# Optimization experiments

Measured on AMD Instinct MI355X. Metric: run time of the kernel, lower is better.

Reference implementation:

```python
import jax, jax.numpy as jnp
import numpy as np
import math

B, S, D = 2, 4096, 512
H = 8
DH = D // H  # 64


def setup_inputs() -> dict:
    key = jax.random.key(0)
    k1, k2, k3, k4, k5 = jax.random.split(key, 5)
    scale = 1.0 / math.sqrt(D)
    return {
        "x": jax.random.normal(k1, (B, S, D), dtype=jnp.float32),
        "W_in": jax.random.normal(k2, (D, 3 * D), dtype=jnp.float32) * scale,
        "b_in": jax.random.normal(k3, (3 * D,), dtype=jnp.float32) * 0.01,
        "W_out": jax.random.normal(k4, (D, D), dtype=jnp.float32) * scale,
        "b_out": jax.random.normal(k5, (D,), dtype=jnp.float32) * 0.01,
        "causal_mask": 1,
    }


def reference(x, W_in, b_in, W_out, b_out, causal_mask):
    b, s, d = x.shape
    # fused QKV projection: (b, s, 3d)
    qkv = x @ W_in + b_in
    q, k, v = jnp.split(qkv, 3, axis=-1)
    # (b, s, d) -> (b, h, s, dh)
    def to_heads(t):
        return t.reshape(b, s, H, DH).transpose(0, 2, 1, 3)
    q, k, v = to_heads(q), to_heads(k), to_heads(v)
    # raw scores (b, h, s, s)
    scores = jnp.einsum("bhqd,bhkd->bhqk", q, k)
    if causal_mask:  # static python flag
        # upper-triangular (strictly above diag) -> -inf, applied pre-scaling
        # (matches source; -inf invariant under /sqrt(d_head))
        tri = jnp.triu(jnp.ones((s, s), dtype=bool), k=1)
        scores = jnp.where(tri, -jnp.inf, scores)
    attn = jax.nn.softmax(scores / math.sqrt(DH), axis=-1)
    out = jnp.einsum("bhqk,bhkd->bhqd", attn, v)
    out = out.transpose(0, 2, 1, 3).reshape(b, s, d)
    return out @ W_out + b_out
```

## Files before the change

### kernel.cpp

```cpp
#include <hip/hip_runtime.h>
#include <cstdint>
#include <cmath>

typedef unsigned short BF16;
typedef __attribute__((ext_vector_type(8))) short short8;
typedef __attribute__((ext_vector_type(4))) float f32x4;
typedef __attribute__((ext_vector_type(16))) float f32x16;
typedef __attribute__((ext_vector_type(2))) unsigned int uint2v;
typedef __attribute__((ext_vector_type(4))) unsigned int uint4v;

#define S_LEN 4096
#define DMODEL 512
#define NHEAD 8
#define DHEAD 64
#define BS 2
#define NROWS (BS * NHEAD * S_LEN)

__device__ __forceinline__ BF16 f2bf(float f) {
  union { float f; uint32_t u; } v; v.f = f;
  uint32_t r = (v.u + 0x7FFFu + ((v.u >> 16) & 1u)) >> 16;
  return (BF16)r;
}

__device__ __forceinline__ unsigned cvtpk(float a, float b) {
  unsigned r;
  asm volatile("v_cvt_pk_bf16_f32 %0, %1, %2" : "=v"(r) : "v"(a), "v"(b));
  return r;
}

__device__ __forceinline__ float partner32(float x, int hi) {
  unsigned a = __float_as_uint(x), b = a;
  uint2v r = __builtin_amdgcn_permlane32_swap(a, b, false, false);
  return __uint_as_float(hi ? r[0] : r[1]);
}

__device__ __forceinline__ void pl32(unsigned &a, unsigned &b) {
  uint2v r = __builtin_amdgcn_permlane32_swap(a, b, false, false);
  a = r[0]; b = r[1];
}

__device__ __forceinline__ void gload16(const void* g, void* lds) {
  __builtin_amdgcn_global_load_lds(
      (const __attribute__((address_space(1))) void*)g,
      (__attribute__((address_space(3))) void*)lds, 16, 0, 0);
}

#define MAX3(a, b, c) fmaxf(fmaxf((a), (b)), (c))
#define CS_CONST 0.18033688011112042f

__global__ __launch_bounds__(256) void cvt_x_k(const float* __restrict__ x,
                                               BF16* __restrict__ xb) {
  int i = blockIdx.x * 256 + threadIdx.x;
  float4 v = reinterpret_cast<const float4*>(x)[i];
  ushort4 o;
  o.x = f2bf(v.x); o.y = f2bf(v.y); o.z = f2bf(v.z); o.w = f2bf(v.w);
  reinterpret_cast<ushort4*>(xb)[i] = o;
}

__global__ __launch_bounds__(256) void tr_cvt_k(const float* __restrict__ W,
                                                BF16* __restrict__ Wt,
                                                int K, int N) {
  __shared__ float t[32][33];
  int n0 = blockIdx.x * 32, k0 = blockIdx.y * 32;
  int tx = threadIdx.x & 31, ty = threadIdx.x >> 5;
#pragma unroll
  for (int i = 0; i < 4; ++i)
    t[ty + 8 * i][tx] = W[(size_t)(k0 + ty + 8 * i) * N + n0 + tx];
  __syncthreads();
#pragma unroll
  for (int i = 0; i < 4; ++i)
    Wt[(size_t)(n0 + ty + 8 * i) * K + k0 + tx] = f2bf(t[tx][ty + 8 * i]);
}

template <int MODE>
__global__ __launch_bounds__(256)
void gemm_k(const BF16* __restrict__ A, const BF16* __restrict__ Bt,
            const float* __restrict__ bias,
            BF16* __restrict__ Qb, BF16* __restrict__ Kb, BF16* __restrict__ Vt,
            float* __restrict__ Out) {
  __shared__ BF16 As[128 * 64];
  __shared__ BF16 Bs[128 * 64];
  const int tid = threadIdx.x;
  const int l = tid & 63, w = tid >> 6;
  const int wm = w >> 1, wn = w & 1;
  const int bm = blockIdx.x, bn = blockIdx.y;
  f32x4 acc[4][4] = {};

  for (int kt = 0; kt < 512 / 64; ++kt) {
#pragma unroll
    for (int i = 0; i < 4; ++i) {
      int ldsoff = i * 4096 + w * 1024;
      int off = ldsoff + l * 16;
      int row = off >> 7;
      int slot = ((off >> 4) & 7) ^ (row & 7);
      gload16(A + (size_t)(bm * 128 + row) * 512 + kt * 64 + slot * 8,
              (char*)As + ldsoff);
      gload16(Bt + (size_t)(bn * 128 + row) * 512 + kt * 64 + slot * 8,
              (char*)Bs + ldsoff);
    }
    __syncthreads();
    const char* Ab = (const char*)As;
    const char* Bb = (const char*)Bs;
    short8 af[4][2], bfr[4][2];
#pragma unroll
    for (int mf = 0; mf < 4; ++mf)
#pragma unroll
      for (int kk = 0; kk < 2; ++kk) {
        int row = wm * 64 + mf * 16 + (l & 15);
        int slot = ((l >> 4) + 4 * kk) ^ (row & 7);
        af[mf][kk] = *(const short8*)(Ab + row * 128 + slot * 16);
      }
#pragma unroll
    for (int nf = 0; nf < 4; ++nf)
#pragma unroll
      for (int kk = 0; kk < 2; ++kk) {
        int row = wn * 64 + nf * 16 + (l & 15);
        int slot = ((l >> 4) + 4 * kk) ^ (row & 7);
        bfr[nf][kk] = *(const short8*)(Bb + row * 128 + slot * 16);
      }
    __builtin_amdgcn_s_setprio(1);
#pragma unroll
    for (int kk = 0; kk < 2; ++kk)
#pragma unroll
      for (int mf = 0; mf < 4; ++mf)
#pragma unroll
        for (int nf = 0; nf < 4; ++nf)
          acc[mf][nf] = __builtin_amdgcn_mfma_f32_16x16x32_bf16(
              af[mf][kk], bfr[nf][kk], acc[mf][nf], 0, 0, 0);
    __builtin_amdgcn_s_setprio(0);
    __syncthreads();
  }

#pragma unroll
  for (int mf = 0; mf < 4; ++mf)
#pragma unroll
    for (int nf = 0; nf < 4; ++nf)
#pragma unroll
      for (int r = 0; r < 4; ++r) {
        int row = bm * 128 + wm * 64 + mf * 16 + ((l >> 4) << 2) + r;
        int col = bn * 128 + wn * 64 + nf * 16 + (l & 15);
        float v = acc[mf][nf][r] + bias[col];
        if (MODE == 0) {
          int sec = col >> 9, nl = col & 511;
          int h = nl >> 6, dh = nl & 63;
          int b = row >> 12, s = row & 4095;
          size_t bh = (size_t)(b * NHEAD + h);
          if (sec == 0)
            Qb[(bh * S_LEN + s) * DHEAD + dh] = f2bf(v);
          else if (sec == 1)
            Kb[(bh * S_LEN + s) * DHEAD + dh] = f2bf(v);
          else
            Vt[(bh * DHEAD + dh) * S_LEN + s] = f2bf(v);
        } else {
          Out[(size_t)row * DMODEL + col] = v;
        }
      }
}

__global__ __launch_bounds__(256, 2)
void attn_k(const BF16* __restrict__ Qg, const BF16* __restrict__ Kg,
            const BF16* __restrict__ Vg, float* __restrict__ Op0,
            float* __restrict__ Op1, float* __restrict__ Ml) {
  __shared__ BF16 Kl[2][64 * 64];
  __shared__ BF16 Vl[2][64 * 64];
  const int tid = threadIdx.x, l = tid & 63, w = tid >> 6;
  const int hi = l >> 5, ln = l & 31;
  const int wgid = blockIdx.x;
  const int xcd = wgid & 7, j = wgid >> 3;
  const int bh = xcd * 2 + (j & 1);
  const int half = (j >> 1) & 1;
  const int p = j >> 2;
  const BF16* Qh = Qg + (size_t)bh * S_LEN * DHEAD;
  const BF16* Kh = Kg + (size_t)bh * S_LEN * DHEAD;
  const BF16* Vh = Vg + (size_t)bh * DHEAD * S_LEN;
  const float CS = CS_CONST;

  int cur = 0;
  for (int rep = 0; rep < 2; ++rep) {
    const int qt = rep ? (31 - p) : p;
    const int kbase = half ? (qt + 1) : 0;
    const int NT = qt + 1;
    const int q0w = qt * 128 + w * 32;
    const int qrow = q0w + ln;
    __syncthreads();

    short8 qb[4];
    {
      const BF16* qp = Qh + (size_t)qrow * DHEAD + hi * 8;
#pragma unroll
      for (int ks = 0; ks < 4; ++ks) qb[ks] = *(const short8*)(qp + ks * 16);
    }
    f32x16 oacc0 = {}, oacc1 = {};
    float m_ = -INFINITY, l_ = 0.f;

    auto stage = [&](int buf, int ktile) {
      const int kv0 = ktile * 64;
#pragma unroll
      for (int i = 0; i < 2; ++i) {
        int base = i * 4096 + w * 1024;
        int off = base + l * 16;
        int row = off >> 7;
        int slot = ((off >> 4) & 7) ^ (row & 7);
        gload16(Kh + (size_t)(kv0 + row) * DHEAD + slot * 8, (char*)Kl[buf] + base);
        gload16(Vh + (size_t)row * S_LEN + kv0 + slot * 8, (char*)Vl[buf] + base);
      }
    };
    stage(cur, kbase);

    for (int kt = 0; kt < NT; ++kt) {
      __syncthreads();
      if (kt + 1 < NT) stage(cur ^ 1, kbase + kt + 1);
      const int kv0 = (kbase + kt) * 64;
      if (kv0 <= q0w + 31) {
        const char* Kb_ = (const char*)Kl[cur];
        f32x16 s0 = {}, s1 = {};
        __builtin_amdgcn_s_setprio(1);
#pragma unroll
        for (int ks = 0; ks < 4; ++ks) {
          int slot0 = (2 * ks + hi) ^ (ln & 7);
          short8 kf0 = *(const short8*)(Kb_ + ln * 128 + slot0 * 16);
          int row1 = 32 + ln;
          int slot1 = (2 * ks + hi) ^ (row1 & 7);
          short8 kf1 = *(const short8*)(Kb_ + row1 * 128 + slot1 * 16);
          s0 = __builtin_amdgcn_mfma_f32_32x32x16_bf16(kf0, qb[ks], s0, 0, 0, 0);
          s1 = __builtin_amdgcn_mfma_f32_32x32x16_bf16(kf1, qb[ks], s1, 0, 0, 0);
        }
        __builtin_amdgcn_s_setprio(0);
        if (kv0 + 63 > q0w) {
#pragma unroll
          for (int r = 0; r < 16; ++r) {
            int crow = (r & 3) + 8 * (r >> 2) + 4 * hi;
            if (kv0 + crow > qrow) s0[r] = -INFINITY;
            if (kv0 + 32 + crow > qrow) s1[r] = -INFINITY;
          }
        }
        float a0 = MAX3(s0[0], s0[1], s0[2]);
        float a1 = MAX3(s0[3], s0[4], s0[5]);
        float a2 = MAX3(s0[6], s0[7], s0[8]);
        float a3 = MAX3(s0[9], s0[10], s0[11]);
        float a4 = MAX3(s0[12], s0[13], s0[14]);
        float a5 = MAX3(s0[15], s1[0], s1[1]);
        float a6 = MAX3(s1[2], s1[3], s1[4]);
        float a7 = MAX3(s1[5], s1[6], s1[7]);
        float a8 = MAX3(s1[8], s1[9], s1[10]);
        float a9 = MAX3(s1[11], s1[12], s1[13]);
        float a10 = fmaxf(s1[14], s1[15]);
        float b0 = MAX3(a0, a1, a2);
        float b1 = MAX3(a3, a4, a5);
        float b2 = MAX3(a6, a7, a8);
        float b3 = fmaxf(a9, a10);
        float pmax = fmaxf(fmaxf(b0, b1), fmaxf(b2, b3));
        pmax = fmaxf(pmax, partner32(pmax, hi));
        bool need = (pmax - m_) * CS > 8.0f;
        if (__any(need)) {
          float mn = fmaxf(m_, pmax);
          float alpha = exp2f((m_ - mn) * CS);
          m_ = mn;
          l_ *= alpha;
#pragma unroll
          for (int r = 0; r < 16; ++r) { oacc0[r] *= alpha; oacc1[r] *= alpha; }
        }
        const float mb = m_ * CS;
        float p0[16], p1[16];
        float rs = 0.f;
#pragma unroll
        for (int r = 0; r < 16; ++r) { p0[r] = exp2f(fmaf(s0[r], CS, -mb)); rs += p0[r]; }
#pragma unroll
        for (int r = 0; r < 16; ++r) { p1[r] = exp2f(fmaf(s1[r], CS, -mb)); rs += p1[r]; }
        rs += partner32(rs, hi);
        l_ += rs;
        short8 pf[4];
#pragma unroll
        for (int hf = 0; hf < 2; ++hf) {
          const float* pp = hf ? p1 : p0;
          unsigned w01 = cvtpk(pp[0], pp[1]), w23 = cvtpk(pp[2], pp[3]);
          unsigned w45 = cvtpk(pp[4], pp[5]), w67 = cvtpk(pp[6], pp[7]);
          unsigned w89 = cvtpk(pp[8], pp[9]), wab = cvtpk(pp[10], pp[11]);
          unsigned wcd = cvtpk(pp[12], pp[13]), wef = cvtpk(pp[14], pp[15]);
          pl32(w01, w45);
          pl32(w23, w67);
          pl32(w89, wcd);
          pl32(wab, wef);
          union { uint4v u; short8 s; } c0, c1;
          c0.u = (uint4v){w01, w23, w45, w67};
          c1.u = (uint4v){w89, wab, wcd, wef};
          pf[hf * 2 + 0] = c0.s;
          pf[hf * 2 + 1] = c1.s;
        }
        const char* Vb_ = (const char*)Vl[cur];
        __builtin_amdgcn_s_setprio(1);
#pragma unroll
        for (int ks = 0; ks < 4; ++ks) {
          int slot0 = (2 * ks + hi) ^ (ln & 7);
          short8 vf0 = *(const short8*)(Vb_ + ln * 128 + slot0 * 16);
          int row1 = 32 + ln;
          int slot1 = (2 * ks + hi) ^ (row1 & 7);
          short8 vf1 = *(const short8*)(Vb_ + row1 * 128 + slot1 * 16);
          oacc0 = __builtin_amdgcn_mfma_f32_32x32x16_bf16(vf0, pf[ks], oacc0, 0, 0, 0);
          oacc1 = __builtin_amdgcn_mfma_f32_32x32x16_bf16(vf1, pf[ks], oacc1, 0, 0, 0);
        }
        __builtin_amdgcn_s_setprio(0);
      }
      cur ^= 1;
    }

    float* Op = half ? Op1 : Op0;
    const size_t rowbase = ((size_t)bh * S_LEN + qrow) * DHEAD;
#pragma unroll
    for (int blk = 0; blk < 2; ++blk) {
      const f32x16 oa = blk ? oacc1 : oacc0;
#pragma unroll
      for (int g = 0; g < 4; ++g) {
        int dh0 = 8 * g + 4 * hi + 32 * blk;
        float4 st = {oa[4 * g + 0], oa[4 * g + 1], oa[4 * g + 2], oa[4 * g + 3]};
        *(float4*)(Op + rowbase + dh0) = st;
      }
    }
    if (hi == 0) {
      float2 ml = {m_, l_};
      *(float2*)(Ml + ((size_t)half * NROWS + (size_t)bh * S_LEN + qrow) * 2) = ml;
    }
  }
}

__global__ __launch_bounds__(256)
void merge_k(const float* __restrict__ Op0, const float* __restrict__ Op1,
             const float* __restrict__ Ml, BF16* __restrict__ Ob) {
  const int wv = blockIdx.x * 4 + (threadIdx.x >> 6);
  const int lane = threadIdx.x & 63;
  const int row0 = wv * 64;
  for (int r = 0; r < 64; ++r) {
    int row = row0 + r;
    float2 ml1 = *(const float2*)(Ml + (size_t)row * 2);
    float2 ml2 = *(const float2*)(Ml + ((size_t)NROWS + row) * 2);
    float m = fmaxf(ml1.x, ml2.x);
    float a1 = exp2f((ml1.x - m) * CS_CONST);
    float a2 = exp2f((ml2.x - m) * CS_CONST);
    float linv = 1.0f / (ml1.y * a1 + ml2.y * a2);
    float o = (Op0[(size_t)row * 64 + lane] * a1 +
               Op1[(size_t)row * 64 + lane] * a2) * linv;
    int bh = row >> 12, s = row & 4095;
    Ob[((size_t)((bh >> 3) * S_LEN + s)) * DMODEL + (bh & 7) * DHEAD + lane] = f2bf(o);
  }
}

extern "C" void kernel_launch(void* const* d_in, const int* in_sizes, int n_in,
                              void* d_out, int out_size, void* d_ws, size_t ws_size,
                              hipStream_t stream) {
  const float* x = (const float*)d_in[0];
  const float* W_in = (const float*)d_in[1];
  const float* b_in = (const float*)d_in[2];
  const float* W_out = (const float*)d_in[3];
  const float* b_out = (const float*)d_in[4];
  float* out = (float*)d_out;

  char* ws = (char*)d_ws;
  const size_t SZ_X = (size_t)BS * S_LEN * DMODEL * 2;
  const size_t SZ_OP = (size_t)NROWS * DHEAD * 4;
  BF16* xb    = (BF16*)(ws);
  BF16* wint  = (BF16*)(ws + SZ_X);
  BF16* woutt = (BF16*)(ws + SZ_X + 3 * DMODEL * DMODEL * 2);
  BF16* Qb    = (BF16*)(ws + SZ_X + 4 * DMODEL * DMODEL * 2);
  BF16* Kb    = (BF16*)((char*)Qb + SZ_X);
  BF16* Vt    = (BF16*)((char*)Kb + SZ_X);
  BF16* Ob    = (BF16*)((char*)Vt + SZ_X);
  float* Op0  = (float*)((char*)Ob + SZ_X);
  float* Op1  = (float*)((char*)Op0 + SZ_OP);
  float* Ml   = (float*)((char*)Op1 + SZ_OP);

  cvt_x_k<<<dim3((BS * S_LEN * DMODEL) / 4 / 256), 256, 0, stream>>>(x, xb);
  tr_cvt_k<<<dim3(3 * DMODEL / 32, DMODEL / 32), 256, 0, stream>>>(W_in, wint, DMODEL, 3 * DMODEL);
  tr_cvt_k<<<dim3(DMODEL / 32, DMODEL / 32), 256, 0, stream>>>(W_out, woutt, DMODEL, DMODEL);
  gemm_k<0><<<dim3(BS * S_LEN / 128, 3 * DMODEL / 128), 256, 0, stream>>>(
      xb, wint, b_in, Qb, Kb, Vt, nullptr);
  attn_k<<<dim3(512), 256, 0, stream>>>(Qb, Kb, Vt, Op0, Op1, Ml);
  merge_k<<<dim3(256), 256, 0, stream>>>(Op0, Op1, Ml, Ob);
  gemm_k<1><<<dim3(BS * S_LEN / 128, DMODEL / 128), 256, 0, stream>>>(
      Ob, woutt, b_out, nullptr, nullptr, nullptr, out);
}
```

Baseline: 209.4 us.

## Split attention KV range four ways, store bf16 partials, raise occupancy

Attention work per query tile is now split over four KV ranges instead of two, doubling the grid to 1024 workgroups and raising the launch-bounds occupancy hint to 4. Partial outputs are stored as bf16 instead of fp32, and the merge kernel combines four partials using their per-slice max and sum. The aim is better load balance and more parallelism across CUs, plus less partial-output traffic. In exchange there are more Q reloads and partial writes, added merge work, bf16 rounding of unnormalized partials, and possible register pressure or spills under the tighter occupancy bound.

```diff
diff --git a/kernel.cpp b/kernel.cpp
--- a/kernel.cpp
+++ b/kernel.cpp
@@ -157,10 +157,10 @@
       }
 }
 
-__global__ __launch_bounds__(256, 2)
+__global__ __launch_bounds__(256, 4)
 void attn_k(const BF16* __restrict__ Qg, const BF16* __restrict__ Kg,
-            const BF16* __restrict__ Vg, float* __restrict__ Op0,
-            float* __restrict__ Op1, float* __restrict__ Ml) {
+            const BF16* __restrict__ Vg, BF16* __restrict__ Opb,
+            float* __restrict__ Ml) {
   __shared__ BF16 Kl[2][64 * 64];
   __shared__ BF16 Vl[2][64 * 64];
   const int tid = threadIdx.x, l = tid & 63, w = tid >> 6;
@@ -168,8 +168,8 @@
   const int wgid = blockIdx.x;
   const int xcd = wgid & 7, j = wgid >> 3;
   const int bh = xcd * 2 + (j & 1);
-  const int half = (j >> 1) & 1;
-  const int p = j >> 2;
+  const int qr = (j >> 1) & 3;
+  const int p = j >> 3;
   const BF16* Qh = Qg + (size_t)bh * S_LEN * DHEAD;
   const BF16* Kh = Kg + (size_t)bh * S_LEN * DHEAD;
   const BF16* Vh = Vg + (size_t)bh * DHEAD * S_LEN;
@@ -178,8 +178,11 @@
   int cur = 0;
   for (int rep = 0; rep < 2; ++rep) {
     const int qt = rep ? (31 - p) : p;
-    const int kbase = half ? (qt + 1) : 0;
-    const int NT = qt + 1;
+    const int qq = rep ? (3 - qr) : qr;
+    const int NTf = 2 * qt + 2;
+    const int kbase = (qq * NTf) >> 2;
+    const int kend = ((qq + 1) * NTf) >> 2;
+    const int NT = kend - kbase;
     const int q0w = qt * 128 + w * 32;
     const int qrow = q0w + ln;
     __syncthreads();
@@ -205,140 +208,153 @@
         gload16(Vh + (size_t)row * S_LEN + kv0 + slot * 8, (char*)Vl[buf] + base);
       }
     };
-    stage(cur, kbase);
-
-    for (int kt = 0; kt < NT; ++kt) {
-      __syncthreads();
-      if (kt + 1 < NT) stage(cur ^ 1, kbase + kt + 1);
-      const int kv0 = (kbase + kt) * 64;
-      if (kv0 <= q0w + 31) {
-        const char* Kb_ = (const char*)Kl[cur];
-        f32x16 s0 = {}, s1 = {};
-        __builtin_amdgcn_s_setprio(1);
-#pragma unroll
-        for (int ks = 0; ks < 4; ++ks) {
-          int slot0 = (2 * ks + hi) ^ (ln & 7);
-          short8 kf0 = *(const short8*)(Kb_ + ln * 128 + slot0 * 16);
-          int row1 = 32 + ln;
-          int slot1 = (2 * ks + hi) ^ (row1 & 7);
-          short8 kf1 = *(const short8*)(Kb_ + row1 * 128 + slot1 * 16);
-          s0 = __builtin_amdgcn_mfma_f32_32x32x16_bf16(kf0, qb[ks], s0, 0, 0, 0);
-          s1 = __builtin_amdgcn_mfma_f32_32x32x16_bf16(kf1, qb[ks], s1, 0, 0, 0);
+
+    if (NT > 0) {
+      stage(cur, kbase);
+      for (int kt = 0; kt < NT; ++kt) {
+        __syncthreads();
+        if (kt + 1 < NT) stage(cur ^ 1, kbase + kt + 1);
+        const int kv0 = (kbase + kt) * 64;
+        if (kv0 <= q0w + 31) {
+          const char* Kb_ = (const char*)Kl[cur];
+          f32x16 s0 = {}, s1 = {};
+          __builtin_amdgcn_s_setprio(1);
+#pragma unroll
+          for (int ks = 0; ks < 4; ++ks) {
+            int slot0 = (2 * ks + hi) ^ (ln & 7);
+            short8 kf0 = *(const short8*)(Kb_ + ln * 128 + slot0 * 16);
+            int row1 = 32 + ln;
+            int slot1 = (2 * ks + hi) ^ (row1 & 7);
+            short8 kf1 = *(const short8*)(Kb_ + row1 * 128 + slot1 * 16);
+            s0 = __builtin_amdgcn_mfma_f32_32x32x16_bf16(kf0, qb[ks], s0, 0, 0, 0);
+            s1 = __builtin_amdgcn_mfma_f32_32x32x16_bf16(kf1, qb[ks], s1, 0, 0, 0);
+          }
+          __builtin_amdgcn_s_setprio(0);
+          if (kv0 + 63 > q0w) {
+#pragma unroll
+            for (int r = 0; r < 16; ++r) {
+              int crow = (r & 3) + 8 * (r >> 2) + 4 * hi;
+              if (kv0 + crow > qrow) s0[r] = -INFINITY;
+              if (kv0 + 32 + crow > qrow) s1[r] = -INFINITY;
+            }
+          }
+          float a0 = MAX3(s0[0], s0[1], s0[2]);
+          float a1 = MAX3(s0[3], s0[4], s0[5]);
+          float a2 = MAX3(s0[6], s0[7], s0[8]);
+          float a3 = MAX3(s0[9], s0[10], s0[11]);
+          float a4 = MAX3(s0[12], s0[13], s0[14]);
+          float a5 = MAX3(s0[15], s1[0], s1[1]);
+          float a6 = MAX3(s1[2], s1[3], s1[4]);
+          float a7 = MAX3(s1[5], s1[6], s1[7]);
+          float a8 = MAX3(s1[8], s1[9], s1[10]);
+          float a9 = MAX3(s1[11], s1[12], s1[13]);
+          float a10 = fmaxf(s1[14], s1[15]);
+          float b0 = MAX3(a0, a1, a2);
+          float b1 = MAX3(a3, a4, a5);
+          float b2 = MAX3(a6, a7, a8);
+          float b3 = fmaxf(a9, a10);
+          float pmax = fmaxf(fmaxf(b0, b1), fmaxf(b2, b3));
+          pmax = fmaxf(pmax, partner32(pmax, hi));
+          bool need = (pmax - m_) * CS > 8.0f;
+          if (__any(need)) {
+            float mn = fmaxf(m_, pmax);
+            float alpha = exp2f((m_ - mn) * CS);
+            m_ = mn;
+            l_ *= alpha;
+#pragma unroll
+            for (int r = 0; r < 16; ++r) { oacc0[r] *= alpha; oacc1[r] *= alpha; }
+          }
+          const float mb = m_ * CS;
+          float p0[16], p1[16];
+          float rs = 0.f;
+#pragma unroll
+          for (int r = 0; r < 16; ++r) { p0[r] = exp2f(fmaf(s0[r], CS, -mb)); rs += p0[r]; }
+#pragma unroll
+          for (int r = 0; r < 16; ++r) { p1[r] = exp2f(fmaf(s1[r], CS, -mb)); rs += p1[r]; }
+          rs += partner32(rs, hi);
+          l_ += rs;
+          short8 pf[4];
+#pragma unroll
+          for (int hf = 0; hf < 2; ++hf) {
+            const float* pp = hf ? p1 : p0;
+            unsigned w01 = cvtpk(pp[0], pp[1]), w23 = cvtpk(pp[2], pp[3]);
+            unsigned w45 = cvtpk(pp[4], pp[5]), w67 = cvtpk(pp[6], pp[7]);
+            unsigned w89 = cvtpk(pp[8], pp[9]), wab = cvtpk(pp[10], pp[11]);
+            unsigned wcd = cvtpk(pp[12], pp[13]), wef = cvtpk(pp[14], pp[15]);
+            pl32(w01, w45);
+            pl32(w23, w67);
+            pl32(w89, wcd);
+            pl32(wab, wef);
+            union { uint4v u; short8 s; } c0, c1;
+            c0.u = (uint4v){w01, w23, w45, w67};
+            c1.u = (uint4v){w89, wab, wcd, wef};
+            pf[hf * 2 + 0] = c0.s;
+            pf[hf * 2 + 1] = c1.s;
+          }
+          const char* Vb_ = (const char*)Vl[cur];
+          __builtin_amdgcn_s_setprio(1);
+#pragma unroll
+          for (int ks = 0; ks < 4; ++ks) {
+            int slot0 = (2 * ks + hi) ^ (ln & 7);
+            short8 vf0 = *(const short8*)(Vb_ + ln * 128 + slot0 * 16);
+            int row1 = 32 + ln;
+            int slot1 = (2 * ks + hi) ^ (row1 & 7);
+            short8 vf1 = *(const short8*)(Vb_ + row1 * 128 + slot1 * 16);
+            oacc0 = __builtin_amdgcn_mfma_f32_32x32x16_bf16(vf0, pf[ks], oacc0, 0, 0, 0);
+            oacc1 = __builtin_amdgcn_mfma_f32_32x32x16_bf16(vf1, pf[ks], oacc1, 0, 0, 0);
+          }
+          __builtin_amdgcn_s_setprio(0);
         }
-        __builtin_amdgcn_s_setprio(0);
-        if (kv0 + 63 > q0w) {
-#pragma unroll
-          for (int r = 0; r < 16; ++r) {
-            int crow = (r & 3) + 8 * (r >> 2) + 4 * hi;
-            if (kv0 + crow > qrow) s0[r] = -INFINITY;
-            if (kv0 + 32 + crow > qrow) s1[r] = -INFINITY;
-          }
-        }
-        float a0 = MAX3(s0[0], s0[1], s0[2]);
-        float a1 = MAX3(s0[3], s0[4], s0[5]);
-        float a2 = MAX3(s0[6], s0[7], s0[8]);
-        float a3 = MAX3(s0[9], s0[10], s0[11]);
-        float a4 = MAX3(s0[12], s0[13], s0[14]);
-        float a5 = MAX3(s0[15], s1[0], s1[1]);
-        float a6 = MAX3(s1[2], s1[3], s1[4]);
-        float a7 = MAX3(s1[5], s1[6], s1[7]);
-        float a8 = MAX3(s1[8], s1[9], s1[10]);
-        float a9 = MAX3(s1[11], s1[12], s1[13]);
-        float a10 = fmaxf(s1[14], s1[15]);
-        float b0 = MAX3(a0, a1, a2);
-        float b1 = MAX3(a3, a4, a5);
-        float b2 = MAX3(a6, a7, a8);
-        float b3 = fmaxf(a9, a10);
-        float pmax = fmaxf(fmaxf(b0, b1), fmaxf(b2, b3));
-        pmax = fmaxf(pmax, partner32(pmax, hi));
-        bool need = (pmax - m_) * CS > 8.0f;
-        if (__any(need)) {
-          float mn = fmaxf(m_, pmax);
-          float alpha = exp2f((m_ - mn) * CS);
-          m_ = mn;
-          l_ *= alpha;
-#pragma unroll
-          for (int r = 0; r < 16; ++r) { oacc0[r] *= alpha; oacc1[r] *= alpha; }
-        }
-        const float mb = m_ * CS;
-        float p0[16], p1[16];
-        float rs = 0.f;
-#pragma unroll
-        for (int r = 0; r < 16; ++r) { p0[r] = exp2f(fmaf(s0[r], CS, -mb)); rs += p0[r]; }
-#pragma unroll
-        for (int r = 0; r < 16; ++r) { p1[r] = exp2f(fmaf(s1[r], CS, -mb)); rs += p1[r]; }
-        rs += partner32(rs, hi);
-        l_ += rs;
-        short8 pf[4];
-#pragma unroll
-        for (int hf = 0; hf < 2; ++hf) {
-          const float* pp = hf ? p1 : p0;
-          unsigned w01 = cvtpk(pp[0], pp[1]), w23 = cvtpk(pp[2], pp[3]);
-          unsigned w45 = cvtpk(pp[4], pp[5]), w67 = cvtpk(pp[6], pp[7]);
-          unsigned w89 = cvtpk(pp[8], pp[9]), wab = cvtpk(pp[10], pp[11]);
-          unsigned wcd = cvtpk(pp[12], pp[13]), wef = cvtpk(pp[14], pp[15]);
-          pl32(w01, w45);
-          pl32(w23, w67);
-          pl32(w89, wcd);
-          pl32(wab, wef);
-          union { uint4v u; short8 s; } c0, c1;
-          c0.u = (uint4v){w01, w23, w45, w67};
-          c1.u = (uint4v){w89, wab, wcd, wef};
-          pf[hf * 2 + 0] = c0.s;
-          pf[hf * 2 + 1] = c1.s;
-        }
-        const char* Vb_ = (const char*)Vl[cur];
-        __builtin_amdgcn_s_setprio(1);
-#pragma unroll
-        for (int ks = 0; ks < 4; ++ks) {
-          int slot0 = (2 * ks + hi) ^ (ln & 7);
-          short8 vf0 = *(const short8*)(Vb_ + ln * 128 + slot0 * 16);
-          int row1 = 32 + ln;
-          int slot1 = (2 * ks + hi) ^ (row1 & 7);
-          short8 vf1 = *(const short8*)(Vb_ + row1 * 128 + slot1 * 16);
-          oacc0 = __builtin_amdgcn_mfma_f32_32x32x16_bf16(vf0, pf[ks], oacc0, 0, 0, 0);
-          oacc1 = __builtin_amdgcn_mfma_f32_32x32x16_bf16(vf1, pf[ks], oacc1, 0, 0, 0);
-        }
-        __builtin_amdgcn_s_setprio(0);
-      }
-      cur ^= 1;
-    }
-
-    float* Op = half ? Op1 : Op0;
-    const size_t rowbase = ((size_t)bh * S_LEN + qrow) * DHEAD;
+        cur ^= 1;
+      }
+    }
+
+    BF16* Op = Opb + ((size_t)qq * NROWS + (size_t)bh * S_LEN + qrow) * DHEAD;
 #pragma unroll
     for (int blk = 0; blk < 2; ++blk) {
       const f32x16 oa = blk ? oacc1 : oacc0;
 #pragma unroll
       for (int g = 0; g < 4; ++g) {
         int dh0 = 8 * g + 4 * hi + 32 * blk;
-        float4 st = {oa[4 * g + 0], oa[4 * g + 1], oa[4 * g + 2], oa[4 * g + 3]};
-        *(float4*)(Op + rowbase + dh0) = st;
+        unsigned lo = cvtpk(oa[4 * g + 0], oa[4 * g + 1]);
+        unsigned h2 = cvtpk(oa[4 * g + 2], oa[4 * g + 3]);
+        uint2v st = {lo, h2};
+        *(uint2v*)(Op + dh0) = st;
       }
     }
     if (hi == 0) {
       float2 ml = {m_, l_};
-      *(float2*)(Ml + ((size_t)half * NROWS + (size_t)bh * S_LEN + qrow) * 2) = ml;
+      *(float2*)(Ml + ((size_t)qq * NROWS + (size_t)bh * S_LEN + qrow) * 2) = ml;
     }
   }
 }
 
 __global__ __launch_bounds__(256)
-void merge_k(const float* __restrict__ Op0, const float* __restrict__ Op1,
-             const float* __restrict__ Ml, BF16* __restrict__ Ob) {
+void merge_k(const BF16* __restrict__ Opb, const float* __restrict__ Ml,
+             BF16* __restrict__ Ob) {
   const int wv = blockIdx.x * 4 + (threadIdx.x >> 6);
   const int lane = threadIdx.x & 63;
   const int row0 = wv * 64;
   for (int r = 0; r < 64; ++r) {
     int row = row0 + r;
-    float2 ml1 = *(const float2*)(Ml + (size_t)row * 2);
-    float2 ml2 = *(const float2*)(Ml + ((size_t)NROWS + row) * 2);
-    float m = fmaxf(ml1.x, ml2.x);
+    float2 ml0 = *(const float2*)(Ml + (size_t)row * 2);
+    float2 ml1 = *(const float2*)(Ml + ((size_t)NROWS + row) * 2);
+    float2 ml2 = *(const float2*)(Ml + ((size_t)2 * NROWS + row) * 2);
+    float2 ml3 = *(const float2*)(Ml + ((size_t)3 * NROWS + row) * 2);
+    float m = fmaxf(fmaxf(ml0.x, ml1.x), fmaxf(ml2.x, ml3.x));
+    float a0 = exp2f((ml0.x - m) * CS_CONST);
     float a1 = exp2f((ml1.x - m) * CS_CONST);
     float a2 = exp2f((ml2.x - m) * CS_CONST);
-    float linv = 1.0f / (ml1.y * a1 + ml2.y * a2);
-    float o = (Op0[(size_t)row * 64 + lane] * a1 +
-               Op1[(size_t)row * 64 + lane] * a2) * linv;
+    float a3 = exp2f((ml3.x - m) * CS_CONST);
+    float linv = 1.0f / (ml0.y * a0 + ml1.y * a1 + ml2.y * a2 + ml3.y * a3);
+    union { unsigned short u; } t;
+    auto ld = [&](int slot) -> float {
+      unsigned short u = Opb[((size_t)slot * NROWS + row) * DHEAD + lane];
+      unsigned x = ((unsigned)u) << 16;
+      return __uint_as_float(x);
+    };
+    float o = (ld(0) * a0 + ld(1) * a1 + ld(2) * a2 + ld(3) * a3) * linv;
+    (void)t;
     int bh = row >> 12, s = row & 4095;
     Ob[((size_t)((bh >> 3) * S_LEN + s)) * DMODEL + (bh & 7) * DHEAD + lane] = f2bf(o);
   }
@@ -356,7 +372,7 @@
 
   char* ws = (char*)d_ws;
   const size_t SZ_X = (size_t)BS * S_LEN * DMODEL * 2;
-  const size_t SZ_OP = (size_t)NROWS * DHEAD * 4;
+  const size_t SZ_OP = (size_t)NROWS * DHEAD * 2;
   BF16* xb    = (BF16*)(ws);
   BF16* wint  = (BF16*)(ws + SZ_X);
   BF16* woutt = (BF16*)(ws + SZ_X + 3 * DMODEL * DMODEL * 2);
@@ -364,17 +380,16 @@
   BF16* Kb    = (BF16*)((char*)Qb + SZ_X);
   BF16* Vt    = (BF16*)((char*)Kb + SZ_X);
   BF16* Ob    = (BF16*)((char*)Vt + SZ_X);
-  float* Op0  = (float*)((char*)Ob + SZ_X);
-  float* Op1  = (float*)((char*)Op0 + SZ_OP);
-  float* Ml   = (float*)((char*)Op1 + SZ_OP);
+  BF16* Opb   = (BF16*)((char*)Ob + SZ_X);
+  float* Ml   = (float*)((char*)Opb + 4 * SZ_OP);
 
   cvt_x_k<<<dim3((BS * S_LEN * DMODEL) / 4 / 256), 256, 0, stream>>>(x, xb);
   tr_cvt_k<<<dim3(3 * DMODEL / 32, DMODEL / 32), 256, 0, stream>>>(W_in, wint, DMODEL, 3 * DMODEL);
   tr_cvt_k<<<dim3(DMODEL / 32, DMODEL / 32), 256, 0, stream>>>(W_out, woutt, DMODEL, DMODEL);
   gemm_k<0><<<dim3(BS * S_LEN / 128, 3 * DMODEL / 128), 256, 0, stream>>>(
       xb, wint, b_in, Qb, Kb, Vt, nullptr);
-  attn_k<<<dim3(512), 256, 0, stream>>>(Qb, Kb, Vt, Op0, Op1, Ml);
-  merge_k<<<dim3(256), 256, 0, stream>>>(Op0, Op1, Ml, Ob);
+  attn_k<<<dim3(1024), 256, 0, stream>>>(Qb, Kb, Vt, Opb, Ml);
+  merge_k<<<dim3(256), 256, 0, stream>>>(Opb, Ml, Ob);
   gemm_k<1><<<dim3(BS * S_LEN / 128, DMODEL / 128), 256, 0, stream>>>(
       Ob, woutt, b_out, nullptr, nullptr, nullptr, out);
 }
```

Measured after the change: 215.1 us. 1.03x slower.
